# Kernel optimization log

Hardware: AMD Instinct MI355X
Metric: run time of the kernel (lower is better)

The kernel has to match this reference:

```python
import jax, jax.numpy as jnp
import numpy as np

B, TMAX = 16, 30
FEAT = 512   # feat_chans
RNN = 512    # rnn_units == embedding_units (required by the module's wiring)
ATTN = 512   # attention_units
VOCAB = 110  # vocab_size; embedding/output have VOCAB+1 entries
H, W = 8, 64


def setup_inputs() -> dict:
    key = jax.random.key(0)
    ks = jax.random.split(key, 20)
    s = 0.02
    G = 4 * RNN
    return {
        "features": jax.random.normal(ks[0], (B, FEAT, H, W), jnp.float32),
        "encoded": jax.random.normal(ks[1], (B, RNN), jnp.float32),
        # embedding table: (vocab_size + 1, embedding_units)
        "embed_w": jax.random.normal(ks[2], (VOCAB + 1, RNN), jnp.float32) * s,
        # decoder LSTMCell(embedding_units, rnn_units)
        "dec_Wih": jax.random.normal(ks[3], (G, RNN), jnp.float32) * s,
        "dec_Whh": jax.random.normal(ks[4], (G, RNN), jnp.float32) * s,
        "dec_bih": jnp.zeros((G,), jnp.float32),
        "dec_bhh": jnp.zeros((G,), jnp.float32),
        # attention LSTMCell(feat_chans, rnn_units)
        "att_Wih": jax.random.normal(ks[5], (G, FEAT), jnp.float32) * s,
        "att_Whh": jax.random.normal(ks[6], (G, RNN), jnp.float32) * s,
        "att_bih": jnp.zeros((G,), jnp.float32),
        "att_bhh": jnp.zeros((G,), jnp.float32),
        # feat_conv: Conv2d(feat_chans, attention_units, 3, padding='same')
        "feat_conv_w": jax.random.normal(ks[7], (ATTN, FEAT, 3, 3), jnp.float32) * s,
        "feat_conv_b": jnp.zeros((ATTN,), jnp.float32),
        # state_conv: Conv2d(rnn_units, attention_units, 1, bias=False) -> plain matmul on [B,RNN]
        "state_conv_w": jax.random.normal(ks[8], (ATTN, RNN), jnp.float32) * s,
        # attention_projector: Conv2d(attention_units, 1, 1, bias=False)
        "attn_proj_w": jax.random.normal(ks[9], (ATTN,), jnp.float32) * s,
        # output_dense: Linear(rnn_units, vocab_size + 1)
        "out_w": jax.random.normal(ks[10], (VOCAB + 1, RNN), jnp.float32) * s,
        "out_b": jnp.zeros((VOCAB + 1,), jnp.float32),
        "gt": jax.random.randint(ks[11], (B, TMAX), 0, VOCAB + 1),
    }


def _lstm_cell(x, h, c, Wih, Whh, bih, bhh):
    # PyTorch LSTMCell gate order: i, f, g, o
    gates = x @ Wih.T + bih + h @ Whh.T + bhh
    i, f, g, o = jnp.split(gates, 4, axis=-1)
    c_new = jax.nn.sigmoid(f) * c + jax.nn.sigmoid(i) * jnp.tanh(g)
    h_new = jax.nn.sigmoid(o) * jnp.tanh(c_new)
    return h_new, c_new


def reference(features, encoded, embed_w, dec_Wih, dec_Whh, dec_bih, dec_bhh,
              att_Wih, att_Whh, att_bih, att_bhh,
              feat_conv_w, feat_conv_b, state_conv_w, attn_proj_w,
              out_w, out_b, gt):
    b = features.shape[0]
    hdim = features.shape[2] * features.shape[3]
    zeros = jnp.zeros((b, dec_Whh.shape[1]), features.dtype)
    # decoder LSTM: zero initial state on both calls (second call also omits state)
    h0, c0 = _lstm_cell(encoded, zeros, zeros, dec_Wih, dec_Whh, dec_bih, dec_bhh)
    # (the second decoder lstm call produces hidden_state/cell_state which are
    #  never used downstream, so it does not affect the output)

    # feat_conv is applied to constant features -> hoist out of the time loop
    feat_proj = jax.lax.conv_general_dilated(
        features, feat_conv_w, (1, 1), 'SAME',
        dimension_numbers=('NCHW', 'OIHW', 'NCHW')) + feat_conv_b[None, :, None, None]

    emb = embed_w[gt]  # [B, T, E] teacher-forcing embeddings

    def step(_, emb_t):
        h1, c1 = _lstm_cell(emb_t, h0, c0, att_Wih, att_Whh, att_bih, att_bhh)
        h2, _ = _lstm_cell(h0, h1, c1, att_Wih, att_Whh, att_bih, att_bhh)
        state_proj = h2 @ state_conv_w.T  # [B, ATTN] (1x1 conv on 1x1 map)
        a = jnp.tanh(feat_proj + state_proj[:, :, None, None])  # [B, ATTN, H, W]
        scores = jnp.einsum('bahw,a->bhw', a, attn_proj_w)  # 1x1 conv to 1 chan
        attn = jax.nn.softmax(scores.reshape(b, hdim), axis=-1)
        attn = attn.reshape(scores.shape)
        glimpse = jnp.einsum('bchw,bhw->bc', features, attn)  # [B, FEAT]
        logits = glimpse @ out_w.T + out_b  # dropout with p=0 is identity
        return None, logits

    _, outs = jax.lax.scan(step, None, jnp.swapaxes(emb, 0, 1))  # [T, B, V+1]
    return jnp.swapaxes(outs, 0, 1)  # [B, T, V+1]
```

## Files before the change

kernel.cpp:

```cpp
#include <hip/hip_runtime.h>
#include <hip/hip_bf16.h>
#include <stdint.h>

#define BB 16
#define TMAX 30
#define FEAT 512
#define RNN 512
#define ATTN 512
#define VOCABP1 111
#define HWD 512
#define PH 10
#define PW 66
#define PROWS 660
#define G4 2048
#define NHC 16
#define LSTR 40

typedef unsigned short u16;
typedef __attribute__((ext_vector_type(8))) unsigned short us8v;
typedef __attribute__((ext_vector_type(8))) short short8;
typedef __attribute__((ext_vector_type(4))) float f32x4;

__device__ __forceinline__ float b2f(u16 b){
  unsigned int u = ((unsigned int)b) << 16;
  return __builtin_bit_cast(float, u);
}
__device__ __forceinline__ u16 f2b(float x){
  unsigned int u = __builtin_bit_cast(unsigned int, x);
  unsigned int r = u + 0x7FFFu + ((u >> 16) & 1u);
  return (u16)(r >> 16);
}
__device__ __forceinline__ float fsig(float x){ return __fdividef(1.0f, 1.0f + __expf(-x)); }
__device__ __forceinline__ float ftanhf(float x){ return 1.0f - __fdividef(2.0f, __expf(2.0f*x) + 1.0f); }

__global__ __launch_bounds__(256) void k_prep(const float* __restrict__ feats, const float* __restrict__ fconv_w,
                                              const float* __restrict__ att_Wih, const float* __restrict__ att_Whh,
                                              const float* __restrict__ scw, const float* __restrict__ embw,
                                              u16* __restrict__ featsP, u16* __restrict__ wB,
                                              u16* __restrict__ wAih, u16* __restrict__ wAhh,
                                              u16* __restrict__ wScw, u16* __restrict__ wEmb){
  __shared__ float tile[64*65];
  int blk = blockIdx.x, tid = threadIdx.x;
  if (blk < 1024){
    int hwb = blk & 7, cb = (blk >> 3) & 7, b = blk >> 6;
    int c0 = cb*64, hw0 = hwb*64;
    int tx = tid & 63, ty = tid >> 6;
#pragma unroll
    for (int r = 0; r < 16; ++r){
      int cl = ty*16 + r;
      tile[cl*65 + tx] = feats[((size_t)(b*FEAT + c0 + cl))*HWD + hw0 + tx];
    }
    __syncthreads();
#pragma unroll
    for (int r = 0; r < 16; ++r){
      int hwl = ty*16 + r;
      int hw = hw0 + hwl;
      int rowP = hw + 2*(hw >> 6) + 67;
      featsP[((size_t)b*PROWS + rowP)*FEAT + c0 + tx] = f2b(tile[tx*65 + hwl]);
    }
  } else if (blk < 2048){
    int idx = (blk - 1024)*256 + tid;
#pragma unroll
    for (int j = 0; j < 9; ++j){
      int e = j*262144 + idx;
      int c = e & 511, n = (e >> 9) & 511, k9 = e >> 18;
      wB[e] = f2b(fconv_w[((size_t)(n*512 + c))*9 + k9]);
    }
  } else if (blk < 2560){
    const int T2 = 1048576 + 1048576 + 262144 + VOCABP1*512;
    int gtid = (blk - 2048)*256 + tid;
    for (int e = gtid; e < T2; e += 131072){
      if (e < 1048576)            wAih[e]           = f2b(att_Wih[e]);
      else if (e < 2097152)       wAhh[e - 1048576] = f2b(att_Whh[e - 1048576]);
      else if (e < 2359296)       wScw[e - 2097152] = f2b(scw[e - 2097152]);
      else                        wEmb[e - 2359296] = f2b(embw[e - 2359296]);
    }
  } else {
    int blkl = blk - 2560;
    for (int r = blkl; r < 148*BB; r += 128){
      int b = r / 148, j = r % 148;
      int rowP;
      if (j < 66) rowP = j;
      else if (j < 132) rowP = 594 + (j - 66);
      else if (j < 140) rowP = (j - 132 + 1)*66;
      else rowP = (j - 140 + 1)*66 + 65;
      ((unsigned int*)&featsP[((size_t)b*PROWS + rowP)*FEAT])[tid] = 0u;
    }
  }
}

__global__ __launch_bounds__(256) void k_conv(const u16* __restrict__ featsP, const u16* __restrict__ wB,
                                              const float* __restrict__ bias, float* __restrict__ fpe){
  __shared__ __align__(16) u16 As[128*LSTR];
  __shared__ __align__(16) u16 Bs[64*LSTR];
  int m0 = blockIdx.x * 128, n0 = blockIdx.y * 64;
  int tid = threadIdx.x, lane = tid & 63, wave = tid >> 6;
  int wm = wave >> 1, wn = wave & 1;

  int kk = (lane & 3) * 8;
  int rA0 = 32*wave + (lane >> 2);
  int rA1 = rA0 + 16;
  int mA0 = m0 + rA0, mA1 = m0 + rA1;
  long baseA0 = ((long)((mA0 >> 9)*PH + ((mA0 >> 6) & 7) + 1)*PW + (mA0 & 63) + 1)*FEAT + kk;
  long baseA1 = ((long)((mA1 >> 9)*PH + ((mA1 >> 6) & 7) + 1)*PW + (mA1 & 63) + 1)*FEAT + kk;
  int nloc = 16*wave + (lane >> 2);
  long baseB = (long)(n0 + nloc)*512 + kk;

  f32x4 acc[4][2];
#pragma unroll
  for (int i=0;i<4;++i)
#pragma unroll
    for (int j=0;j<2;++j) acc[i][j] = (f32x4){0.f,0.f,0.f,0.f};

  int arow = wm*64 + (lane & 15);
  int akc  = (lane >> 4) * 8;
  int brow = wn*32 + (lane & 15);

  us8v a0c, a1c, bc;
  {
    long dA = (long)(-1*PW - 1)*FEAT;
    a0c = *(const us8v*)(featsP + baseA0 + dA);
    a1c = *(const us8v*)(featsP + baseA1 + dA);
    bc  = *(const us8v*)(wB + baseB);
  }

  for (int ks = 0; ks < 144; ++ks){
    __syncthreads();
    *(us8v*)&As[rA0*LSTR + kk] = a0c;
    *(us8v*)&As[rA1*LSTR + kk] = a1c;
    *(us8v*)&Bs[nloc*LSTR + kk] = bc;
    __syncthreads();
    if (ks < 143){
      int kn = ks + 1;
      int o = kn >> 4;
      int c0 = (kn & 15) << 5;
      int dy = o/3 - 1, dx = o - (o/3)*3 - 1;
      long dA = (long)(dy*PW + dx)*FEAT + c0;
      long dB = (long)o*(512*512) + c0;
      a0c = *(const us8v*)(featsP + baseA0 + dA);
      a1c = *(const us8v*)(featsP + baseA1 + dA);
      bc  = *(const us8v*)(wB + baseB + dB);
    }
    short8 a[4], bfr[2];
#pragma unroll
    for (int mt=0; mt<4; ++mt) a[mt] = *(const short8*)&As[(arow + mt*16)*LSTR + akc];
#pragma unroll
    for (int nt=0; nt<2; ++nt) bfr[nt] = *(const short8*)&Bs[(brow + nt*16)*LSTR + akc];
#pragma unroll
    for (int mt=0; mt<4; ++mt)
#pragma unroll
      for (int nt=0; nt<2; ++nt)
        acc[mt][nt] = __builtin_amdgcn_mfma_f32_16x16x32_bf16(a[mt], bfr[nt], acc[mt][nt], 0, 0, 0);
  }
  int col = lane & 15;
  int rbase = (lane >> 4) * 4;
#pragma unroll
  for (int mt=0; mt<4; ++mt){
#pragma unroll
    for (int nt=0; nt<2; ++nt){
      int gn = n0 + wn*32 + nt*16 + col;
      float bv = bias[gn];
#pragma unroll
      for (int r=0; r<4; ++r){
        int gm = m0 + wm*64 + mt*16 + rbase + r;
        fpe[(size_t)gm*ATTN + gn] = __expf(2.0f*(acc[mt][nt][r] + bv));
      }
    }
  }
}

template<int MODE, bool EXPOUT>
__global__ __launch_bounds__(256) void k_gemm_mfma(const u16* __restrict__ A, const u16* __restrict__ X,
                                                   const int* __restrict__ gt, float* __restrict__ G, int M){
  __shared__ __align__(16) u16 As[128*LSTR];
  __shared__ __align__(16) u16 Bs[64*LSTR];
  int m0 = blockIdx.x * 128, n0 = blockIdx.y * 64;
  int tid = threadIdx.x, lane = tid & 63, wave = tid >> 6;
  int wm = wave >> 1, wn = wave & 1;

  int kk = (lane & 3) * 8;
  int rA0 = 32*wave + (lane >> 2);
  int rA1 = rA0 + 16;
  const u16* aptr0 = A + (size_t)(m0 + rA0)*512 + kk;
  const u16* aptr1 = A + (size_t)(m0 + rA1)*512 + kk;
  int nloc = 16*wave + (lane >> 2);
  int btc = n0 + nloc; if (btc > 479) btc = 479;
  const u16* bptr;
  if (MODE == 0) bptr = X + (size_t)gt[btc]*512 + kk;
  else           bptr = X + (size_t)btc*512 + kk;

  f32x4 acc[4][2];
#pragma unroll
  for (int i=0;i<4;++i)
#pragma unroll
    for (int j=0;j<2;++j) acc[i][j] = (f32x4){0.f,0.f,0.f,0.f};

  int arow = wm*64 + (lane & 15);
  int akc  = (lane >> 4) * 8;
  int brow = wn*32 + (lane & 15);

  us8v a0c = *(const us8v*)aptr0;
  us8v a1c = *(const us8v*)aptr1;
  us8v bc  = *(const us8v*)bptr;

  for (int ks = 0; ks < 16; ++ks){
    __syncthreads();
    *(us8v*)&As[rA0*LSTR + kk] = a0c;
    *(us8v*)&As[rA1*LSTR + kk] = a1c;
    *(us8v*)&Bs[nloc*LSTR + kk] = bc;
    __syncthreads();
    if (ks < 15){
      int off = (ks + 1)*32;
      a0c = *(const us8v*)(aptr0 + off);
      a1c = *(const us8v*)(aptr1 + off);
      bc  = *(const us8v*)(bptr + off);
    }
    short8 a[4], bfr[2];
#pragma unroll
    for (int mt=0; mt<4; ++mt) a[mt] = *(const short8*)&As[(arow + mt*16)*LSTR + akc];
#pragma unroll
    for (int nt=0; nt<2; ++nt) bfr[nt] = *(const short8*)&Bs[(brow + nt*16)*LSTR + akc];
#pragma unroll
    for (int mt=0; mt<4; ++mt)
#pragma unroll
      for (int nt=0; nt<2; ++nt)
        acc[mt][nt] = __builtin_amdgcn_mfma_f32_16x16x32_bf16(a[mt], bfr[nt], acc[mt][nt], 0, 0, 0);
  }
  int col = lane & 15;
  int rbase = (lane >> 4) * 4;
#pragma unroll
  for (int mt=0; mt<4; ++mt){
#pragma unroll
    for (int nt=0; nt<2; ++nt){
      int gbt = n0 + wn*32 + nt*16 + col;
      if (gbt < 480){
#pragma unroll
        for (int r=0; r<4; ++r){
          int gm = m0 + wm*64 + mt*16 + rbase + r;
          float v = acc[mt][nt][r];
          if (EXPOUT) v = __expf(2.0f*v);
          G[(size_t)gbt*M + gm] = v;
        }
      }
    }
  }
}

__global__ __launch_bounds__(256) void k_dec_gemm(const float* __restrict__ encoded, const float* __restrict__ Wih,
                                                  float* __restrict__ Gd){
  __shared__ float encL[512][16];
  int m0 = blockIdx.x * 64;
  int tid = threadIdx.x;
  for (int p = 0; p < 2; ++p){
    int k = p*256 + tid;
    for (int n = 0; n < 16; ++n) encL[k][n] = encoded[n*512 + k];
  }
  __syncthreads();
  int m_l = tid & 63, ng = tid >> 6;
  float acc[4] = {0.f,0.f,0.f,0.f};
  const float* wrow = Wih + (size_t)(m0 + m_l)*512;
  for (int k = 0; k < 512; k += 4){
    float4 w4 = *(const float4*)&wrow[k];
#pragma unroll
    for (int i=0;i<4;++i){
      int n = ng*4 + i;
      acc[i] += w4.x*encL[k][n] + w4.y*encL[k+1][n] + w4.z*encL[k+2][n] + w4.w*encL[k+3][n];
    }
  }
#pragma unroll
  for (int i=0;i<4;++i) Gd[(size_t)(ng*4+i)*G4 + m0 + m_l] = acc[i];
}

__global__ __launch_bounds__(256) void k_pre_gemm(const float* __restrict__ Gd,
                                                  const float* __restrict__ dbih, const float* __restrict__ dbhh,
                                                  const float* __restrict__ Wih, const float* __restrict__ Whh,
                                                  const float* __restrict__ bih, const float* __restrict__ bhh,
                                                  float* __restrict__ g1h, float* __restrict__ g2x){
  __shared__ float hL[512][16];
  int m0 = blockIdx.x * 64;
  int tid = threadIdx.x;
  for (int i = tid; i < 8192; i += 256){
    int k = i >> 4, n = i & 15;
    float gi = Gd[(size_t)n*G4 + k]        + dbih[k]      + dbhh[k];
    float gg = Gd[(size_t)n*G4 + k + 1024] + dbih[k+1024] + dbhh[k+1024];
    float go = Gd[(size_t)n*G4 + k + 1536] + dbih[k+1536] + dbhh[k+1536];
    float cv = fsig(gi)*ftanhf(gg);
    hL[k][n] = fsig(go)*ftanhf(cv);
  }
  __syncthreads();
  int m_l = tid & 63, ng = tid >> 6;
  int m = m0 + m_l;
  float a1[4] = {0.f,0.f,0.f,0.f}, a2[4] = {0.f,0.f,0.f,0.f};
  const float* w1 = Whh + (size_t)m*512;
  const float* w2 = Wih + (size_t)m*512;
  for (int k = 0; k < 512; k += 4){
    float4 v1 = *(const float4*)&w1[k];
    float4 v2 = *(const float4*)&w2[k];
#pragma unroll
    for (int i=0;i<4;++i){
      int n = ng*4 + i;
      float x0 = hL[k][n], x1 = hL[k+1][n], x2 = hL[k+2][n], x3 = hL[k+3][n];
      a1[i] += v1.x*x0 + v1.y*x1 + v1.z*x2 + v1.w*x3;
      a2[i] += v2.x*x0 + v2.y*x1 + v2.z*x2 + v2.w*x3;
    }
  }
  float bb = bih[m] + bhh[m];
#pragma unroll
  for (int i=0;i<4;++i){
    g1h[(size_t)(ng*4+i)*G4 + m] = a1[i] + bb;
    g2x[(size_t)(ng*4+i)*G4 + m] = a2[i] + bb;
  }
}

__global__ __launch_bounds__(512) void k_lstm1(const float* __restrict__ G1, const float* __restrict__ g1h,
                                               const float* __restrict__ Gd,
                                               const float* __restrict__ dbih, const float* __restrict__ dbhh,
                                               u16* __restrict__ h1b, float* __restrict__ c1){
  int bt = blockIdx.x, b = bt / TMAX, u = threadIdx.x;
  float dgi = Gd[(size_t)b*G4 + u]        + dbih[u]      + dbhh[u];
  float dgg = Gd[(size_t)b*G4 + u + 1024] + dbih[u+1024] + dbhh[u+1024];
  float c0v = fsig(dgi)*ftanhf(dgg);
  float gi_ = G1[(size_t)bt*G4 + u]        + g1h[(size_t)b*G4 + u];
  float gf  = G1[(size_t)bt*G4 + u + 512]  + g1h[(size_t)b*G4 + u + 512];
  float gg  = G1[(size_t)bt*G4 + u + 1024] + g1h[(size_t)b*G4 + u + 1024];
  float go  = G1[(size_t)bt*G4 + u + 1536] + g1h[(size_t)b*G4 + u + 1536];
  float cv = fsig(gf)*c0v + fsig(gi_)*ftanhf(gg);
  float hv = fsig(go)*ftanhf(cv);
  h1b[(size_t)bt*RNN + u] = f2b(hv); c1[(size_t)bt*RNN + u] = cv;
}
__global__ __launch_bounds__(512) void k_lstm2(const float* __restrict__ G2, const float* __restrict__ g2x,
                                               const float* __restrict__ c1, u16* __restrict__ h2b){
  int bt = blockIdx.x, b = bt / TMAX, u = threadIdx.x;
  float gi_ = G2[(size_t)bt*G4 + u]        + g2x[(size_t)b*G4 + u];
  float gf  = G2[(size_t)bt*G4 + u + 512]  + g2x[(size_t)b*G4 + u + 512];
  float gg  = G2[(size_t)bt*G4 + u + 1024] + g2x[(size_t)b*G4 + u + 1024];
  float go  = G2[(size_t)bt*G4 + u + 1536] + g2x[(size_t)b*G4 + u + 1536];
  float cv = fsig(gf)*c1[(size_t)bt*RNN+u] + fsig(gi_)*ftanhf(gg);
  float hv = fsig(go)*ftanhf(cv);
  h2b[(size_t)bt*RNN + u] = f2b(hv);
}

__global__ __launch_bounds__(512) void k_sc(const float* __restrict__ fpe, const float* __restrict__ spe,
                                            const float* __restrict__ apw, float* __restrict__ sc){
  __shared__ float spL[8][516];
  __shared__ float w2L[512];
  int b = blockIdx.x, hw0 = blockIdx.y * 32, t0 = blockIdx.z * 8;
  int tid = threadIdx.x, lane = tid & 63, wave = tid >> 6;
  for (int i = tid; i < 8*512; i += 512){
    int t = i >> 9, a = i & 511;
    int tg = t0 + t;
    spL[t][a] = (tg < TMAX) ? spe[((size_t)(b*TMAX + tg))*ATTN + a] : 0.f;
  }
  w2L[tid] = -2.0f * apw[tid];
  __syncthreads();
#pragma unroll
  for (int r = 0; r < 4; ++r){
    int row = hw0 + wave*4 + r;
    const float* frow = fpe + ((size_t)b*HWD + row)*ATTN;
    float acc[8];
#pragma unroll
    for (int t=0;t<8;++t) acc[t] = 0.f;
#pragma unroll
    for (int a0 = 0; a0 < 8; ++a0){
      int a = a0*64 + lane;
      float ef = frow[a];
      float w2 = w2L[a];
#pragma unroll
      for (int t=0;t<8;++t){
        float d = __builtin_fmaf(ef, spL[t][a], 1.0f);
        acc[t] = __builtin_fmaf(w2, __builtin_amdgcn_rcpf(d), acc[t]);
      }
    }
#pragma unroll
    for (int t=0;t<8;++t){
      float s = acc[t];
#pragma unroll
      for (int off = 32; off; off >>= 1) s += __shfl_xor(s, off);
      if (lane == 0 && (t0 + t) < TMAX) sc[((size_t)(b*TMAX + t0 + t))*HWD + row] = s;
    }
  }
}

__global__ __launch_bounds__(256) void k_smax(const float* __restrict__ sc, float* __restrict__ attn){
  __shared__ float red[256];
  int bt = blockIdx.x, tid = threadIdx.x;
  float v0 = sc[(size_t)bt*HWD + tid], v1 = sc[(size_t)bt*HWD + tid + 256];
  red[tid] = fmaxf(v0, v1); __syncthreads();
  for (int sd=128; sd; sd>>=1){ if (tid < sd) red[tid] = fmaxf(red[tid], red[tid+sd]); __syncthreads(); }
  float mx = red[0]; __syncthreads();
  float e0 = __expf(v0-mx), e1 = __expf(v1-mx);
  red[tid] = e0+e1; __syncthreads();
  for (int sd=128; sd; sd>>=1){ if (tid < sd) red[tid] += red[tid+sd]; __syncthreads(); }
  float inv = __fdividef(1.0f, red[0]);
  attn[(size_t)bt*HWD + tid]     = e0*inv;
  attn[(size_t)bt*HWD + tid+256] = e1*inv;
}

__global__ __launch_bounds__(512) void k_glimpse(const float* __restrict__ attn, const u16* __restrict__ featsP,
                                                 float* __restrict__ gpart){
  __shared__ float atL[TMAX][32];
  int b = blockIdx.x, hc = blockIdx.y;
  int hw0 = hc*32;
  int tid = threadIdx.x;
  for (int i = tid; i < TMAX*32; i += 512){
    int t = i >> 5, hw = i & 31;
    atL[t][hw] = attn[((size_t)(b*TMAX + t))*HWD + hw0 + hw];
  }
  __syncthreads();
  float acc[TMAX];
#pragma unroll
  for (int t=0;t<TMAX;++t) acc[t] = 0.f;
  const u16* fb = featsP + (size_t)b*PROWS*FEAT;
  for (int hw = 0; hw < 32; ++hw){
    int hwg = hw0 + hw;
    int rowP = hwg + 2*(hwg >> 6) + 67;
    float f = b2f(fb[(size_t)rowP*FEAT + tid]);
#pragma unroll
    for (int t=0;t<TMAX;++t) acc[t] = __builtin_fmaf(f, atL[t][hw], acc[t]);
  }
#pragma unroll
  for (int t = 0; t < TMAX; ++t)
    gpart[(((size_t)hc*BB + b)*TMAX + t)*FEAT + tid] = acc[t];
}

__global__ __launch_bounds__(512) void k_logits(const float* __restrict__ gpart,
                                                const float* __restrict__ outw, const float* __restrict__ outb,
                                                float* __restrict__ out){
  __shared__ float gl[512];
  __shared__ float part[4][128];
  int bt = blockIdx.x, b = bt / TMAX, t = bt % TMAX;
  int tid = threadIdx.x;
  float g = 0.f;
#pragma unroll
  for (int p = 0; p < NHC; ++p)
    g += gpart[(((size_t)p*BB + b)*TMAX + t)*FEAT + tid];
  gl[tid] = g;
  __syncthreads();
  int vg = tid >> 7, v = tid & 127;
  int vv = v < VOCABP1 ? v : VOCABP1-1;
  const float* wr = outw + (size_t)vv*512 + vg*128;
  float s = 0.f;
  for (int k = 0; k < 128; k += 4){
    float4 w4 = *(const float4*)&wr[k];
    s += w4.x*gl[vg*128+k] + w4.y*gl[vg*128+k+1] + w4.z*gl[vg*128+k+2] + w4.w*gl[vg*128+k+3];
  }
  part[vg][v] = s;
  __syncthreads();
  if (tid < VOCABP1)
    out[(size_t)bt*VOCABP1 + tid] = part[0][tid] + part[1][tid] + part[2][tid] + part[3][tid] + outb[tid];
}

extern "C" void kernel_launch(void* const* d_in, const int* in_sizes, int n_in,
                              void* d_out, int out_size, void* d_ws, size_t ws_size,
                              hipStream_t stream){
  (void)in_sizes; (void)n_in; (void)out_size; (void)ws_size;
  const float* features = (const float*)d_in[0];
  const float* encoded  = (const float*)d_in[1];
  const float* embed_w  = (const float*)d_in[2];
  const float* dec_Wih  = (const float*)d_in[3];
  const float* dec_bih  = (const float*)d_in[5];
  const float* dec_bhh  = (const float*)d_in[6];
  const float* att_Wih  = (const float*)d_in[7];
  const float* att_Whh  = (const float*)d_in[8];
  const float* att_bih  = (const float*)d_in[9];
  const float* att_bhh  = (const float*)d_in[10];
  const float* fconv_w  = (const float*)d_in[11];
  const float* fconv_b  = (const float*)d_in[12];
  const float* scw      = (const float*)d_in[13];
  const float* apw      = (const float*)d_in[14];
  const float* outw     = (const float*)d_in[15];
  const float* outb     = (const float*)d_in[16];
  const int* gt         = (const int*)d_in[17];

  char* ws = (char*)d_ws;
  u16*  featsP = (u16*)(ws + 0);
  u16*  wB     = (u16*)(ws + 10813440);
  float* fpe   = (float*)(ws + 15532032);
  u16*  wAih   = (u16*)(ws + 32309248);
  u16*  wAhh   = (u16*)(ws + 34406400);
  u16*  wScw   = (u16*)(ws + 36503552);
  u16*  wEmb   = (u16*)(ws + 37027840);
  float* Gd    = (float*)(ws + 37141504);
  float* g1h   = (float*)(ws + 37272576);
  float* g2x   = (float*)(ws + 37403648);
  float* G1    = (float*)(ws + 37534720);
  u16*  h1b    = (u16*)(ws + 41466880);
  float* c1    = (float*)(ws + 41958400);
  u16*  h2b    = (u16*)(ws + 42941440);
  float* spe   = (float*)(ws + 43432960);
  float* sc    = (float*)(ws + 44416000);
  float* attn  = (float*)(ws + 45399040);
  float* gpart = fpe;

  k_prep<<<dim3(2688), 256, 0, stream>>>(features, fconv_w, att_Wih, att_Whh, scw, embed_w,
                                         featsP, wB, wAih, wAhh, wScw, wEmb);
  k_conv<<<dim3(64,8), 256, 0, stream>>>(featsP, wB, fconv_b, fpe);

  k_dec_gemm<<<dim3(32), 256, 0, stream>>>(encoded, dec_Wih, Gd);
  k_pre_gemm<<<dim3(32), 256, 0, stream>>>(Gd, dec_bih, dec_bhh, att_Wih, att_Whh, att_bih, att_bhh, g1h, g2x);

  k_gemm_mfma<0,false><<<dim3(16,8), 256, 0, stream>>>(wAih, wEmb, gt, G1, G4);
  k_lstm1<<<dim3(480), 512, 0, stream>>>(G1, g1h, Gd, dec_bih, dec_bhh, h1b, c1);
  k_gemm_mfma<1,false><<<dim3(16,8), 256, 0, stream>>>(wAhh, h1b, nullptr, G1, G4);
  k_lstm2<<<dim3(480), 512, 0, stream>>>(G1, g2x, c1, h2b);
  k_gemm_mfma<1,true><<<dim3(4,8), 256, 0, stream>>>(wScw, h2b, nullptr, spe, ATTN);

  k_sc<<<dim3(16,16,4), 512, 0, stream>>>(fpe, spe, apw, sc);
  k_smax<<<dim3(480), 256, 0, stream>>>(sc, attn);
  k_glimpse<<<dim3(16,NHC), 512, 0, stream>>>(attn, featsP, gpart);
  k_logits<<<dim3(480), 512, 0, stream>>>(gpart, outw, outb, (float*)d_out);
}
```

Before: 365.5 us.

## Fuse LSTM gates into GEMM epilogues and merge tail kernels

Attention-LSTM weights are repacked into gate-interleaved, K-concatenated [Wih|Whh] matrices so each LSTM cell becomes one GEMM whose epilogue applies the gate nonlinearities directly. This removes the G1 gate buffers and the separate lstm kernels. The decoder initial-state GEMM moves into the prep kernel, and the conv runs in the same launch as the first LSTM GEMM so the two overlap. Softmax, glimpse and logits are fused into one per-(b,t) kernel, which recomputes the glimpse over all 512 positions per block instead of reusing features across timesteps. LDS stride padding (40 to 32) is dropped, which may add bank conflicts.

```diff
diff --git a/kernel.cpp b/kernel.cpp
--- a/kernel.cpp
+++ b/kernel.cpp
@@ -12,9 +12,6 @@
 #define PH 10
 #define PW 66
 #define PROWS 660
-#define G4 2048
-#define NHC 16
-#define LSTR 40
 
 typedef unsigned short u16;
 typedef __attribute__((ext_vector_type(8))) unsigned short us8v;
@@ -33,22 +30,27 @@
 __device__ __forceinline__ float fsig(float x){ return __fdividef(1.0f, 1.0f + __expf(-x)); }
 __device__ __forceinline__ float ftanhf(float x){ return 1.0f - __fdividef(2.0f, __expf(2.0f*x) + 1.0f); }
 
-__global__ __launch_bounds__(256) void k_prep(const float* __restrict__ feats, const float* __restrict__ fconv_w,
-                                              const float* __restrict__ att_Wih, const float* __restrict__ att_Whh,
-                                              const float* __restrict__ scw, const float* __restrict__ embw,
-                                              u16* __restrict__ featsP, u16* __restrict__ wB,
-                                              u16* __restrict__ wAih, u16* __restrict__ wAhh,
-                                              u16* __restrict__ wScw, u16* __restrict__ wEmb){
+__global__ __launch_bounds__(256) void k_prep(
+    const float* __restrict__ feats, const float* __restrict__ fconv_w,
+    const float* __restrict__ att_Wih, const float* __restrict__ att_Whh,
+    const float* __restrict__ scw, const float* __restrict__ embw,
+    const float* __restrict__ att_bih, const float* __restrict__ att_bhh,
+    const float* __restrict__ encoded, const float* __restrict__ dec_Wih,
+    const float* __restrict__ dec_bih, const float* __restrict__ dec_bhh,
+    u16* __restrict__ featsP, u16* __restrict__ wB,
+    u16* __restrict__ wA1, u16* __restrict__ wA2,
+    u16* __restrict__ wScw, u16* __restrict__ wEmb, float* __restrict__ bsumI,
+    u16* __restrict__ h0b, float* __restrict__ c0){
   __shared__ float tile[64*65];
   int blk = blockIdx.x, tid = threadIdx.x;
   if (blk < 1024){
     int hwb = blk & 7, cb = (blk >> 3) & 7, b = blk >> 6;
-    int c0 = cb*64, hw0 = hwb*64;
+    int c0_ = cb*64, hw0 = hwb*64;
     int tx = tid & 63, ty = tid >> 6;
 #pragma unroll
     for (int r = 0; r < 16; ++r){
       int cl = ty*16 + r;
-      tile[cl*65 + tx] = feats[((size_t)(b*FEAT + c0 + cl))*HWD + hw0 + tx];
+      tile[cl*65 + tx] = feats[((size_t)(b*FEAT + c0_ + cl))*HWD + hw0 + tx];
     }
     __syncthreads();
 #pragma unroll
@@ -56,7 +58,7 @@
       int hwl = ty*16 + r;
       int hw = hw0 + hwl;
       int rowP = hw + 2*(hw >> 6) + 67;
-      featsP[((size_t)b*PROWS + rowP)*FEAT + c0 + tx] = f2b(tile[tx*65 + hwl]);
+      featsP[((size_t)b*PROWS + rowP)*FEAT + c0_ + tx] = f2b(tile[tx*65 + hwl]);
     }
   } else if (blk < 2048){
     int idx = (blk - 1024)*256 + tid;
@@ -67,15 +69,26 @@
       wB[e] = f2b(fconv_w[((size_t)(n*512 + c))*9 + k9]);
     }
   } else if (blk < 2560){
-    const int T2 = 1048576 + 1048576 + 262144 + VOCABP1*512;
     int gtid = (blk - 2048)*256 + tid;
-    for (int e = gtid; e < T2; e += 131072){
-      if (e < 1048576)            wAih[e]           = f2b(att_Wih[e]);
-      else if (e < 2097152)       wAhh[e - 1048576] = f2b(att_Whh[e - 1048576]);
-      else if (e < 2359296)       wScw[e - 2097152] = f2b(scw[e - 2097152]);
-      else                        wEmb[e - 2359296] = f2b(embw[e - 2359296]);
-    }
-  } else {
+    for (int e = gtid; e < 2097152; e += 131072){
+      int mp = e >> 10, k = e & 1023;
+      int u = mp >> 2, g = mp & 3;
+      int row = u + 512*g;
+      if (k < 512){
+        wA1[e] = f2b(att_Wih[(size_t)row*512 + k]);
+        wA2[e] = f2b(att_Whh[(size_t)row*512 + k]);
+      } else {
+        wA1[e] = f2b(att_Whh[(size_t)row*512 + k - 512]);
+        wA2[e] = f2b(att_Wih[(size_t)row*512 + k - 512]);
+      }
+    }
+    for (int e = gtid; e < 262144; e += 131072) wScw[e] = f2b(scw[e]);
+    if (gtid < VOCABP1*512) wEmb[gtid] = f2b(embw[gtid]);
+    if (gtid < 2048){
+      int u = gtid >> 2, g = gtid & 3, row = u + 512*g;
+      bsumI[gtid] = att_bih[row] + att_bhh[row];
+    }
+  } else if (blk < 2688){
     int blkl = blk - 2560;
     for (int r = blkl; r < 148*BB; r += 128){
       int b = r / 148, j = r % 148;
@@ -86,66 +99,221 @@
       else rowP = (j - 140 + 1)*66 + 65;
       ((unsigned int*)&featsP[((size_t)b*PROWS + rowP)*FEAT])[tid] = 0u;
     }
-  }
-}
-
-__global__ __launch_bounds__(256) void k_conv(const u16* __restrict__ featsP, const u16* __restrict__ wB,
-                                              const float* __restrict__ bias, float* __restrict__ fpe){
-  __shared__ __align__(16) u16 As[128*LSTR];
-  __shared__ __align__(16) u16 Bs[64*LSTR];
-  int m0 = blockIdx.x * 128, n0 = blockIdx.y * 64;
+  } else {
+    int b = blk - 2688;
+    for (int i = tid; i < 512; i += 256) tile[i] = encoded[b*512 + i];
+    __syncthreads();
+#pragma unroll
+    for (int p = 0; p < 2; ++p){
+      int u = p*256 + tid;
+      float ai = 0.f, ag = 0.f, ao = 0.f;
+      const float* wi = dec_Wih + (size_t)u*512;
+      const float* wg = dec_Wih + (size_t)(u + 1024)*512;
+      const float* wo = dec_Wih + (size_t)(u + 1536)*512;
+      for (int k = 0; k < 512; k += 4){
+        float x0 = tile[k], x1 = tile[k+1], x2 = tile[k+2], x3 = tile[k+3];
+        float4 a4 = *(const float4*)&wi[k]; ai += a4.x*x0 + a4.y*x1 + a4.z*x2 + a4.w*x3;
+        float4 b4 = *(const float4*)&wg[k]; ag += b4.x*x0 + b4.y*x1 + b4.z*x2 + b4.w*x3;
+        float4 c4 = *(const float4*)&wo[k]; ao += c4.x*x0 + c4.y*x1 + c4.z*x2 + c4.w*x3;
+      }
+      float gi = ai + dec_bih[u]      + dec_bhh[u];
+      float gg = ag + dec_bih[u+1024] + dec_bhh[u+1024];
+      float go = ao + dec_bih[u+1536] + dec_bhh[u+1536];
+      float cv = fsig(gi)*ftanhf(gg);
+      float hv = fsig(go)*ftanhf(cv);
+      c0[b*512 + u] = cv;
+      h0b[b*512 + u] = f2b(hv);
+    }
+  }
+}
+
+__global__ __launch_bounds__(256) void k_conv_gemm1(
+    const u16* __restrict__ featsP, const u16* __restrict__ wB,
+    const float* __restrict__ bias, float* __restrict__ fpe,
+    const u16* __restrict__ wA1, const u16* __restrict__ wEmb,
+    const u16* __restrict__ h0b, const int* __restrict__ gt,
+    const float* __restrict__ bsumI, const float* __restrict__ c0,
+    u16* __restrict__ h1b, float* __restrict__ c1){
+  __shared__ __align__(16) u16 As[128*32];
+  __shared__ __align__(16) u16 Bs[64*32];
+  int blk = blockIdx.x;
   int tid = threadIdx.x, lane = tid & 63, wave = tid >> 6;
   int wm = wave >> 1, wn = wave & 1;
-
-  int kk = (lane & 3) * 8;
+  int kk = (lane & 3)*8;
   int rA0 = 32*wave + (lane >> 2);
   int rA1 = rA0 + 16;
-  int mA0 = m0 + rA0, mA1 = m0 + rA1;
-  long baseA0 = ((long)((mA0 >> 9)*PH + ((mA0 >> 6) & 7) + 1)*PW + (mA0 & 63) + 1)*FEAT + kk;
-  long baseA1 = ((long)((mA1 >> 9)*PH + ((mA1 >> 6) & 7) + 1)*PW + (mA1 & 63) + 1)*FEAT + kk;
   int nloc = 16*wave + (lane >> 2);
-  long baseB = (long)(n0 + nloc)*512 + kk;
-
+  int arow = wm*64 + (lane & 15);
+  int akc  = (lane >> 4)*8;
+  int brow = wn*32 + (lane & 15);
   f32x4 acc[4][2];
 #pragma unroll
   for (int i=0;i<4;++i)
 #pragma unroll
     for (int j=0;j<2;++j) acc[i][j] = (f32x4){0.f,0.f,0.f,0.f};
-
-  int arow = wm*64 + (lane & 15);
-  int akc  = (lane >> 4) * 8;
-  int brow = wn*32 + (lane & 15);
-
-  us8v a0c, a1c, bc;
-  {
-    long dA = (long)(-1*PW - 1)*FEAT;
-    a0c = *(const us8v*)(featsP + baseA0 + dA);
-    a1c = *(const us8v*)(featsP + baseA1 + dA);
-    bc  = *(const us8v*)(wB + baseB);
-  }
-
-  for (int ks = 0; ks < 144; ++ks){
-    __syncthreads();
-    *(us8v*)&As[rA0*LSTR + kk] = a0c;
-    *(us8v*)&As[rA1*LSTR + kk] = a1c;
-    *(us8v*)&Bs[nloc*LSTR + kk] = bc;
-    __syncthreads();
-    if (ks < 143){
-      int kn = ks + 1;
-      int o = kn >> 4;
-      int c0 = (kn & 15) << 5;
-      int dy = o/3 - 1, dx = o - (o/3)*3 - 1;
-      long dA = (long)(dy*PW + dx)*FEAT + c0;
-      long dB = (long)o*(512*512) + c0;
+  int col = lane & 15;
+  int rbase = (lane >> 4)*4;
+
+  if (blk < 512){
+    int m0 = (blk & 63)*128, n0 = (blk >> 6)*64;
+    int mA0 = m0 + rA0, mA1 = m0 + rA1;
+    long baseA0 = ((long)((mA0 >> 9)*PH + ((mA0 >> 6) & 7) + 1)*PW + (mA0 & 63) + 1)*FEAT + kk;
+    long baseA1 = ((long)((mA1 >> 9)*PH + ((mA1 >> 6) & 7) + 1)*PW + (mA1 & 63) + 1)*FEAT + kk;
+    long baseB = (long)(n0 + nloc)*512 + kk;
+    us8v a0c, a1c, bc;
+    {
+      long dA = (long)(-1*PW - 1)*FEAT;
       a0c = *(const us8v*)(featsP + baseA0 + dA);
       a1c = *(const us8v*)(featsP + baseA1 + dA);
-      bc  = *(const us8v*)(wB + baseB + dB);
+      bc  = *(const us8v*)(wB + baseB);
+    }
+    for (int ks = 0; ks < 144; ++ks){
+      __syncthreads();
+      *(us8v*)&As[rA0*32 + kk] = a0c;
+      *(us8v*)&As[rA1*32 + kk] = a1c;
+      *(us8v*)&Bs[nloc*32 + kk] = bc;
+      __syncthreads();
+      if (ks < 143){
+        int kn = ks + 1;
+        int o = kn >> 4;
+        int c0_ = (kn & 15) << 5;
+        int dy = o/3 - 1, dx = o - (o/3)*3 - 1;
+        long dA = (long)(dy*PW + dx)*FEAT + c0_;
+        long dB = (long)o*(512*512) + c0_;
+        a0c = *(const us8v*)(featsP + baseA0 + dA);
+        a1c = *(const us8v*)(featsP + baseA1 + dA);
+        bc  = *(const us8v*)(wB + baseB + dB);
+      }
+      short8 a[4], bfr[2];
+#pragma unroll
+      for (int mt=0; mt<4; ++mt) a[mt] = *(const short8*)&As[(arow + mt*16)*32 + akc];
+#pragma unroll
+      for (int nt=0; nt<2; ++nt) bfr[nt] = *(const short8*)&Bs[(brow + nt*16)*32 + akc];
+#pragma unroll
+      for (int mt=0; mt<4; ++mt)
+#pragma unroll
+        for (int nt=0; nt<2; ++nt)
+          acc[mt][nt] = __builtin_amdgcn_mfma_f32_16x16x32_bf16(a[mt], bfr[nt], acc[mt][nt], 0, 0, 0);
+    }
+#pragma unroll
+    for (int mt=0; mt<4; ++mt){
+#pragma unroll
+      for (int nt=0; nt<2; ++nt){
+        int gn = n0 + wn*32 + nt*16 + col;
+        float bv = bias[gn];
+#pragma unroll
+        for (int r=0; r<4; ++r){
+          int gm = m0 + wm*64 + mt*16 + rbase + r;
+          fpe[(size_t)gm*ATTN + gn] = __expf(2.0f*(acc[mt][nt][r] + bv));
+        }
+      }
+    }
+  } else {
+    int b2 = blk - 512;
+    int m0 = (b2 & 15)*128, n0 = (b2 >> 4)*64;
+    const u16* aptr0 = wA1 + (size_t)(m0 + rA0)*1024 + kk;
+    const u16* aptr1 = wA1 + (size_t)(m0 + rA1)*1024 + kk;
+    int btc = n0 + nloc; if (btc > 479) btc = 479;
+    const u16* bp1 = wEmb + (size_t)gt[btc]*512 + kk;
+    const u16* bp2 = h0b + (size_t)(btc/TMAX)*512 + kk;
+    us8v a0c = *(const us8v*)aptr0;
+    us8v a1c = *(const us8v*)aptr1;
+    us8v bc  = *(const us8v*)bp1;
+    for (int ks = 0; ks < 32; ++ks){
+      __syncthreads();
+      *(us8v*)&As[rA0*32 + kk] = a0c;
+      *(us8v*)&As[rA1*32 + kk] = a1c;
+      *(us8v*)&Bs[nloc*32 + kk] = bc;
+      __syncthreads();
+      if (ks < 31){
+        int kn = ks + 1;
+        int off = kn*32;
+        a0c = *(const us8v*)(aptr0 + off);
+        a1c = *(const us8v*)(aptr1 + off);
+        bc  = (kn < 16) ? *(const us8v*)(bp1 + off) : *(const us8v*)(bp2 + off - 512);
+      }
+      short8 a[4], bfr[2];
+#pragma unroll
+      for (int mt=0; mt<4; ++mt) a[mt] = *(const short8*)&As[(arow + mt*16)*32 + akc];
+#pragma unroll
+      for (int nt=0; nt<2; ++nt) bfr[nt] = *(const short8*)&Bs[(brow + nt*16)*32 + akc];
+#pragma unroll
+      for (int mt=0; mt<4; ++mt)
+#pragma unroll
+        for (int nt=0; nt<2; ++nt)
+          acc[mt][nt] = __builtin_amdgcn_mfma_f32_16x16x32_bf16(a[mt], bfr[nt], acc[mt][nt], 0, 0, 0);
+    }
+#pragma unroll
+    for (int mt=0; mt<4; ++mt){
+#pragma unroll
+      for (int nt=0; nt<2; ++nt){
+        int gbt = n0 + wn*32 + nt*16 + col;
+        if (gbt < 480){
+          int gm0 = m0 + wm*64 + mt*16 + rbase;
+          int u = gm0 >> 2;
+          float4 bs = *(const float4*)&bsumI[gm0];
+          float vi = acc[mt][nt][0] + bs.x;
+          float vf = acc[mt][nt][1] + bs.y;
+          float vg = acc[mt][nt][2] + bs.z;
+          float vo = acc[mt][nt][3] + bs.w;
+          float cp = c0[(gbt/TMAX)*512 + u];
+          float cv = fsig(vf)*cp + fsig(vi)*ftanhf(vg);
+          float hv = fsig(vo)*ftanhf(cv);
+          h1b[(size_t)gbt*512 + u] = f2b(hv);
+          c1[(size_t)gbt*512 + u] = cv;
+        }
+      }
+    }
+  }
+}
+
+__global__ __launch_bounds__(256) void k_gemm_lstm2(
+    const u16* __restrict__ wA2, const u16* __restrict__ h1bsrc, const u16* __restrict__ h0b,
+    const float* __restrict__ bsumI, const float* __restrict__ c1, u16* __restrict__ h2b){
+  __shared__ __align__(16) u16 As[128*32];
+  __shared__ __align__(16) u16 Bs[64*32];
+  int m0 = blockIdx.x*128, n0 = blockIdx.y*64;
+  int tid = threadIdx.x, lane = tid & 63, wave = tid >> 6;
+  int wm = wave >> 1, wn = wave & 1;
+  int kk = (lane & 3)*8;
+  int rA0 = 32*wave + (lane >> 2);
+  int rA1 = rA0 + 16;
+  int nloc = 16*wave + (lane >> 2);
+  const u16* aptr0 = wA2 + (size_t)(m0 + rA0)*1024 + kk;
+  const u16* aptr1 = wA2 + (size_t)(m0 + rA1)*1024 + kk;
+  int btc = n0 + nloc; if (btc > 479) btc = 479;
+  const u16* bp1 = h1bsrc + (size_t)btc*512 + kk;
+  const u16* bp2 = h0b + (size_t)(btc/TMAX)*512 + kk;
+  f32x4 acc[4][2];
+#pragma unroll
+  for (int i=0;i<4;++i)
+#pragma unroll
+    for (int j=0;j<2;++j) acc[i][j] = (f32x4){0.f,0.f,0.f,0.f};
+  int arow = wm*64 + (lane & 15);
+  int akc  = (lane >> 4)*8;
+  int brow = wn*32 + (lane & 15);
+
+  us8v a0c = *(const us8v*)aptr0;
+  us8v a1c = *(const us8v*)aptr1;
+  us8v bc  = *(const us8v*)bp1;
+  for (int ks = 0; ks < 32; ++ks){
+    __syncthreads();
+    *(us8v*)&As[rA0*32 + kk] = a0c;
+    *(us8v*)&As[rA1*32 + kk] = a1c;
+    *(us8v*)&Bs[nloc*32 + kk] = bc;
+    __syncthreads();
+    if (ks < 31){
+      int kn = ks + 1;
+      int off = kn*32;
+      a0c = *(const us8v*)(aptr0 + off);
+      a1c = *(const us8v*)(aptr1 + off);
+      bc  = (kn < 16) ? *(const us8v*)(bp1 + off) : *(const us8v*)(bp2 + off - 512);
     }
     short8 a[4], bfr[2];
 #pragma unroll
-    for (int mt=0; mt<4; ++mt) a[mt] = *(const short8*)&As[(arow + mt*16)*LSTR + akc];
-#pragma unroll
-    for (int nt=0; nt<2; ++nt) bfr[nt] = *(const short8*)&Bs[(brow + nt*16)*LSTR + akc];
+    for (int mt=0; mt<4; ++mt) a[mt] = *(const short8*)&As[(arow + mt*16)*32 + akc];
+#pragma unroll
+    for (int nt=0; nt<2; ++nt) bfr[nt] = *(const short8*)&Bs[(brow + nt*16)*32 + akc];
 #pragma unroll
     for (int mt=0; mt<4; ++mt)
 #pragma unroll
@@ -153,61 +321,61 @@
         acc[mt][nt] = __builtin_amdgcn_mfma_f32_16x16x32_bf16(a[mt], bfr[nt], acc[mt][nt], 0, 0, 0);
   }
   int col = lane & 15;
-  int rbase = (lane >> 4) * 4;
+  int rbase = (lane >> 4)*4;
 #pragma unroll
   for (int mt=0; mt<4; ++mt){
 #pragma unroll
     for (int nt=0; nt<2; ++nt){
-      int gn = n0 + wn*32 + nt*16 + col;
-      float bv = bias[gn];
-#pragma unroll
-      for (int r=0; r<4; ++r){
-        int gm = m0 + wm*64 + mt*16 + rbase + r;
-        fpe[(size_t)gm*ATTN + gn] = __expf(2.0f*(acc[mt][nt][r] + bv));
-      }
-    }
-  }
-}
-
-template<int MODE, bool EXPOUT>
-__global__ __launch_bounds__(256) void k_gemm_mfma(const u16* __restrict__ A, const u16* __restrict__ X,
-                                                   const int* __restrict__ gt, float* __restrict__ G, int M){
-  __shared__ __align__(16) u16 As[128*LSTR];
-  __shared__ __align__(16) u16 Bs[64*LSTR];
-  int m0 = blockIdx.x * 128, n0 = blockIdx.y * 64;
+      int gbt = n0 + wn*32 + nt*16 + col;
+      if (gbt < 480){
+        int gm0 = m0 + wm*64 + mt*16 + rbase;
+        int u = gm0 >> 2;
+        float4 bs = *(const float4*)&bsumI[gm0];
+        float vi = acc[mt][nt][0] + bs.x;
+        float vf = acc[mt][nt][1] + bs.y;
+        float vg = acc[mt][nt][2] + bs.z;
+        float vo = acc[mt][nt][3] + bs.w;
+        float cp = c1[(size_t)gbt*512 + u];
+        float cv = fsig(vf)*cp + fsig(vi)*ftanhf(vg);
+        float hv = fsig(vo)*ftanhf(cv);
+        h2b[(size_t)gbt*512 + u] = f2b(hv);
+      }
+    }
+  }
+}
+
+__global__ __launch_bounds__(256) void k_gemm_spe(const u16* __restrict__ A, const u16* __restrict__ X,
+                                                  float* __restrict__ G){
+  __shared__ __align__(16) u16 As[128*32];
+  __shared__ __align__(16) u16 Bs[64*32];
+  int m0 = blockIdx.x*128, n0 = blockIdx.y*64;
   int tid = threadIdx.x, lane = tid & 63, wave = tid >> 6;
   int wm = wave >> 1, wn = wave & 1;
-
-  int kk = (lane & 3) * 8;
+  int kk = (lane & 3)*8;
   int rA0 = 32*wave + (lane >> 2);
   int rA1 = rA0 + 16;
+  int nloc = 16*wave + (lane >> 2);
   const u16* aptr0 = A + (size_t)(m0 + rA0)*512 + kk;
   const u16* aptr1 = A + (size_t)(m0 + rA1)*512 + kk;
-  int nloc = 16*wave + (lane >> 2);
   int btc = n0 + nloc; if (btc > 479) btc = 479;
-  const u16* bptr;
-  if (MODE == 0) bptr = X + (size_t)gt[btc]*512 + kk;
-  else           bptr = X + (size_t)btc*512 + kk;
-
+  const u16* bptr = X + (size_t)btc*512 + kk;
   f32x4 acc[4][2];
 #pragma unroll
   for (int i=0;i<4;++i)
 #pragma unroll
     for (int j=0;j<2;++j) acc[i][j] = (f32x4){0.f,0.f,0.f,0.f};
-
   int arow = wm*64 + (lane & 15);
-  int akc  = (lane >> 4) * 8;
+  int akc  = (lane >> 4)*8;
   int brow = wn*32 + (lane & 15);
 
   us8v a0c = *(const us8v*)aptr0;
   us8v a1c = *(const us8v*)aptr1;
   us8v bc  = *(const us8v*)bptr;
-
   for (int ks = 0; ks < 16; ++ks){
     __syncthreads();
-    *(us8v*)&As[rA0*LSTR + kk] = a0c;
-    *(us8v*)&As[rA1*LSTR + kk] = a1c;
-    *(us8v*)&Bs[nloc*LSTR + kk] = bc;
+    *(us8v*)&As[rA0*32 + kk] = a0c;
+    *(us8v*)&As[rA1*32 + kk] = a1c;
+    *(us8v*)&Bs[nloc*32 + kk] = bc;
     __syncthreads();
     if (ks < 15){
       int off = (ks + 1)*32;
@@ -217,9 +385,9 @@
     }
     short8 a[4], bfr[2];
 #pragma unroll
-    for (int mt=0; mt<4; ++mt) a[mt] = *(const short8*)&As[(arow + mt*16)*LSTR + akc];
-#pragma unroll
-    for (int nt=0; nt<2; ++nt) bfr[nt] = *(const short8*)&Bs[(brow + nt*16)*LSTR + akc];
+    for (int mt=0; mt<4; ++mt) a[mt] = *(const short8*)&As[(arow + mt*16)*32 + akc];
+#pragma unroll
+    for (int nt=0; nt<2; ++nt) bfr[nt] = *(const short8*)&Bs[(brow + nt*16)*32 + akc];
 #pragma unroll
     for (int mt=0; mt<4; ++mt)
 #pragma unroll
@@ -227,7 +395,7 @@
         acc[mt][nt] = __builtin_amdgcn_mfma_f32_16x16x32_bf16(a[mt], bfr[nt], acc[mt][nt], 0, 0, 0);
   }
   int col = lane & 15;
-  int rbase = (lane >> 4) * 4;
+  int rbase = (lane >> 4)*4;
 #pragma unroll
   for (int mt=0; mt<4; ++mt){
 #pragma unroll
@@ -237,107 +405,11 @@
 #pragma unroll
         for (int r=0; r<4; ++r){
           int gm = m0 + wm*64 + mt*16 + rbase + r;
-          float v = acc[mt][nt][r];
-          if (EXPOUT) v = __expf(2.0f*v);
-          G[(size_t)gbt*M + gm] = v;
+          G[(size_t)gbt*512 + gm] = __expf(2.0f*acc[mt][nt][r]);
         }
       }
     }
   }
-}
-
-__global__ __launch_bounds__(256) void k_dec_gemm(const float* __restrict__ encoded, const float* __restrict__ Wih,
-                                                  float* __restrict__ Gd){
-  __shared__ float encL[512][16];
-  int m0 = blockIdx.x * 64;
-  int tid = threadIdx.x;
-  for (int p = 0; p < 2; ++p){
-    int k = p*256 + tid;
-    for (int n = 0; n < 16; ++n) encL[k][n] = encoded[n*512 + k];
-  }
-  __syncthreads();
-  int m_l = tid & 63, ng = tid >> 6;
-  float acc[4] = {0.f,0.f,0.f,0.f};
-  const float* wrow = Wih + (size_t)(m0 + m_l)*512;
-  for (int k = 0; k < 512; k += 4){
-    float4 w4 = *(const float4*)&wrow[k];
-#pragma unroll
-    for (int i=0;i<4;++i){
-      int n = ng*4 + i;
-      acc[i] += w4.x*encL[k][n] + w4.y*encL[k+1][n] + w4.z*encL[k+2][n] + w4.w*encL[k+3][n];
-    }
-  }
-#pragma unroll
-  for (int i=0;i<4;++i) Gd[(size_t)(ng*4+i)*G4 + m0 + m_l] = acc[i];
-}
-
-__global__ __launch_bounds__(256) void k_pre_gemm(const float* __restrict__ Gd,
-                                                  const float* __restrict__ dbih, const float* __restrict__ dbhh,
-                                                  const float* __restrict__ Wih, const float* __restrict__ Whh,
-                                                  const float* __restrict__ bih, const float* __restrict__ bhh,
-                                                  float* __restrict__ g1h, float* __restrict__ g2x){
-  __shared__ float hL[512][16];
-  int m0 = blockIdx.x * 64;
-  int tid = threadIdx.x;
-  for (int i = tid; i < 8192; i += 256){
-    int k = i >> 4, n = i & 15;
-    float gi = Gd[(size_t)n*G4 + k]        + dbih[k]      + dbhh[k];
-    float gg = Gd[(size_t)n*G4 + k + 1024] + dbih[k+1024] + dbhh[k+1024];
-    float go = Gd[(size_t)n*G4 + k + 1536] + dbih[k+1536] + dbhh[k+1536];
-    float cv = fsig(gi)*ftanhf(gg);
-    hL[k][n] = fsig(go)*ftanhf(cv);
-  }
-  __syncthreads();
-  int m_l = tid & 63, ng = tid >> 6;
-  int m = m0 + m_l;
-  float a1[4] = {0.f,0.f,0.f,0.f}, a2[4] = {0.f,0.f,0.f,0.f};
-  const float* w1 = Whh + (size_t)m*512;
-  const float* w2 = Wih + (size_t)m*512;
-  for (int k = 0; k < 512; k += 4){
-    float4 v1 = *(const float4*)&w1[k];
-    float4 v2 = *(const float4*)&w2[k];
-#pragma unroll
-    for (int i=0;i<4;++i){
-      int n = ng*4 + i;
-      float x0 = hL[k][n], x1 = hL[k+1][n], x2 = hL[k+2][n], x3 = hL[k+3][n];
-      a1[i] += v1.x*x0 + v1.y*x1 + v1.z*x2 + v1.w*x3;
-      a2[i] += v2.x*x0 + v2.y*x1 + v2.z*x2 + v2.w*x3;
-    }
-  }
-  float bb = bih[m] + bhh[m];
-#pragma unroll
-  for (int i=0;i<4;++i){
-    g1h[(size_t)(ng*4+i)*G4 + m] = a1[i] + bb;
-    g2x[(size_t)(ng*4+i)*G4 + m] = a2[i] + bb;
-  }
-}
-
-__global__ __launch_bounds__(512) void k_lstm1(const float* __restrict__ G1, const float* __restrict__ g1h,
-                                               const float* __restrict__ Gd,
-                                               const float* __restrict__ dbih, const float* __restrict__ dbhh,
-                                               u16* __restrict__ h1b, float* __restrict__ c1){
-  int bt = blockIdx.x, b = bt / TMAX, u = threadIdx.x;
-  float dgi = Gd[(size_t)b*G4 + u]        + dbih[u]      + dbhh[u];
-  float dgg = Gd[(size_t)b*G4 + u + 1024] + dbih[u+1024] + dbhh[u+1024];
-  float c0v = fsig(dgi)*ftanhf(dgg);
-  float gi_ = G1[(size_t)bt*G4 + u]        + g1h[(size_t)b*G4 + u];
-  float gf  = G1[(size_t)bt*G4 + u + 512]  + g1h[(size_t)b*G4 + u + 512];
-  float gg  = G1[(size_t)bt*G4 + u + 1024] + g1h[(size_t)b*G4 + u + 1024];
-  float go  = G1[(size_t)bt*G4 + u + 1536] + g1h[(size_t)b*G4 + u + 1536];
-  float cv = fsig(gf)*c0v + fsig(gi_)*ftanhf(gg);
-  float hv = fsig(go)*ftanhf(cv);
-  h1b[(size_t)bt*RNN + u] = f2b(hv); c1[(size_t)bt*RNN + u] = cv;
-}
-__global__ __launch_bounds__(512) void k_lstm2(const float* __restrict__ G2, const float* __restrict__ g2x,
-                                               const float* __restrict__ c1, u16* __restrict__ h2b){
-  int bt = blockIdx.x, b = bt / TMAX, u = threadIdx.x;
-  float gi_ = G2[(size_t)bt*G4 + u]        + g2x[(size_t)b*G4 + u];
-  float gf  = G2[(size_t)bt*G4 + u + 512]  + g2x[(size_t)b*G4 + u + 512];
-  float gg  = G2[(size_t)bt*G4 + u + 1024] + g2x[(size_t)b*G4 + u + 1024];
-  float go  = G2[(size_t)bt*G4 + u + 1536] + g2x[(size_t)b*G4 + u + 1536];
-  float cv = fsig(gf)*c1[(size_t)bt*RNN+u] + fsig(gi_)*ftanhf(gg);
-  float hv = fsig(go)*ftanhf(cv);
-  h2b[(size_t)bt*RNN + u] = f2b(hv);
 }
 
 __global__ __launch_bounds__(512) void k_sc(const float* __restrict__ fpe, const float* __restrict__ spe,
@@ -381,70 +453,53 @@
   }
 }
 
-__global__ __launch_bounds__(256) void k_smax(const float* __restrict__ sc, float* __restrict__ attn){
-  __shared__ float red[256];
-  int bt = blockIdx.x, tid = threadIdx.x;
-  float v0 = sc[(size_t)bt*HWD + tid], v1 = sc[(size_t)bt*HWD + tid + 256];
-  red[tid] = fmaxf(v0, v1); __syncthreads();
-  for (int sd=128; sd; sd>>=1){ if (tid < sd) red[tid] = fmaxf(red[tid], red[tid+sd]); __syncthreads(); }
-  float mx = red[0]; __syncthreads();
-  float e0 = __expf(v0-mx), e1 = __expf(v1-mx);
-  red[tid] = e0+e1; __syncthreads();
-  for (int sd=128; sd; sd>>=1){ if (tid < sd) red[tid] += red[tid+sd]; __syncthreads(); }
-  float inv = __fdividef(1.0f, red[0]);
-  attn[(size_t)bt*HWD + tid]     = e0*inv;
-  attn[(size_t)bt*HWD + tid+256] = e1*inv;
-}
-
-__global__ __launch_bounds__(512) void k_glimpse(const float* __restrict__ attn, const u16* __restrict__ featsP,
-                                                 float* __restrict__ gpart){
-  __shared__ float atL[TMAX][32];
-  int b = blockIdx.x, hc = blockIdx.y;
-  int hw0 = hc*32;
-  int tid = threadIdx.x;
-  for (int i = tid; i < TMAX*32; i += 512){
-    int t = i >> 5, hw = i & 31;
-    atL[t][hw] = attn[((size_t)(b*TMAX + t))*HWD + hw0 + hw];
-  }
-  __syncthreads();
-  float acc[TMAX];
-#pragma unroll
-  for (int t=0;t<TMAX;++t) acc[t] = 0.f;
-  const u16* fb = featsP + (size_t)b*PROWS*FEAT;
-  for (int hw = 0; hw < 32; ++hw){
-    int hwg = hw0 + hw;
-    int rowP = hwg + 2*(hwg >> 6) + 67;
-    float f = b2f(fb[(size_t)rowP*FEAT + tid]);
-#pragma unroll
-    for (int t=0;t<TMAX;++t) acc[t] = __builtin_fmaf(f, atL[t][hw], acc[t]);
-  }
-#pragma unroll
-  for (int t = 0; t < TMAX; ++t)
-    gpart[(((size_t)hc*BB + b)*TMAX + t)*FEAT + tid] = acc[t];
-}
-
-__global__ __launch_bounds__(512) void k_logits(const float* __restrict__ gpart,
-                                                const float* __restrict__ outw, const float* __restrict__ outb,
-                                                float* __restrict__ out){
+__global__ __launch_bounds__(512) void k_tail(const float* __restrict__ sc, const u16* __restrict__ featsP,
+                                              const float* __restrict__ outw, const float* __restrict__ outb,
+                                              float* __restrict__ out){
+  __shared__ float scL[512];
+  __shared__ float red[8];
   __shared__ float gl[512];
   __shared__ float part[4][128];
-  int bt = blockIdx.x, b = bt / TMAX, t = bt % TMAX;
-  int tid = threadIdx.x;
-  float g = 0.f;
-#pragma unroll
-  for (int p = 0; p < NHC; ++p)
-    g += gpart[(((size_t)p*BB + b)*TMAX + t)*FEAT + tid];
-  gl[tid] = g;
-  __syncthreads();
-  int vg = tid >> 7, v = tid & 127;
-  int vv = v < VOCABP1 ? v : VOCABP1-1;
-  const float* wr = outw + (size_t)vv*512 + vg*128;
-  float s = 0.f;
+  int bt = blockIdx.x, b = bt / TMAX;
+  int tid = threadIdx.x, lane = tid & 63, wave = tid >> 6;
+  float v = sc[(size_t)bt*HWD + tid];
+  float m = v;
+#pragma unroll
+  for (int off = 32; off; off >>= 1) m = fmaxf(m, __shfl_xor(m, off));
+  if (lane == 0) red[wave] = m;
+  __syncthreads();
+  float mx = red[0];
+#pragma unroll
+  for (int i = 1; i < 8; ++i) mx = fmaxf(mx, red[i]);
+  float e = __expf(v - mx);
+  float s = e;
+#pragma unroll
+  for (int off = 32; off; off >>= 1) s += __shfl_xor(s, off);
+  __syncthreads();
+  if (lane == 0) red[wave] = s;
+  __syncthreads();
+  float tot = 0.f;
+#pragma unroll
+  for (int i = 0; i < 8; ++i) tot += red[i];
+  scL[tid] = e * __builtin_amdgcn_rcpf(tot);
+  __syncthreads();
+  const u16* fb = featsP + (size_t)b*PROWS*FEAT;
+  float acc = 0.f;
+  for (int hw = 0; hw < HWD; ++hw){
+    int rowP = hw + 2*(hw >> 6) + 67;
+    acc = __builtin_fmaf(b2f(fb[(size_t)rowP*FEAT + tid]), scL[hw], acc);
+  }
+  gl[tid] = acc;
+  __syncthreads();
+  int vg = tid >> 7, vv = tid & 127;
+  int vc = vv < VOCABP1 ? vv : VOCABP1-1;
+  const float* wr = outw + (size_t)vc*512 + vg*128;
+  float so = 0.f;
   for (int k = 0; k < 128; k += 4){
     float4 w4 = *(const float4*)&wr[k];
-    s += w4.x*gl[vg*128+k] + w4.y*gl[vg*128+k+1] + w4.z*gl[vg*128+k+2] + w4.w*gl[vg*128+k+3];
-  }
-  part[vg][v] = s;
+    so += w4.x*gl[vg*128+k] + w4.y*gl[vg*128+k+1] + w4.z*gl[vg*128+k+2] + w4.w*gl[vg*128+k+3];
+  }
+  part[vg][vv] = so;
   __syncthreads();
   if (tid < VOCABP1)
     out[(size_t)bt*VOCABP1 + tid] = part[0][tid] + part[1][tid] + part[2][tid] + part[3][tid] + outb[tid];
@@ -476,37 +531,26 @@
   u16*  featsP = (u16*)(ws + 0);
   u16*  wB     = (u16*)(ws + 10813440);
   float* fpe   = (float*)(ws + 15532032);
-  u16*  wAih   = (u16*)(ws + 32309248);
-  u16*  wAhh   = (u16*)(ws + 34406400);
-  u16*  wScw   = (u16*)(ws + 36503552);
-  u16*  wEmb   = (u16*)(ws + 37027840);
-  float* Gd    = (float*)(ws + 37141504);
-  float* g1h   = (float*)(ws + 37272576);
-  float* g2x   = (float*)(ws + 37403648);
-  float* G1    = (float*)(ws + 37534720);
-  u16*  h1b    = (u16*)(ws + 41466880);
-  float* c1    = (float*)(ws + 41958400);
-  u16*  h2b    = (u16*)(ws + 42941440);
-  float* spe   = (float*)(ws + 43432960);
-  float* sc    = (float*)(ws + 44416000);
-  float* attn  = (float*)(ws + 45399040);
-  float* gpart = fpe;
-
-  k_prep<<<dim3(2688), 256, 0, stream>>>(features, fconv_w, att_Wih, att_Whh, scw, embed_w,
-                                         featsP, wB, wAih, wAhh, wScw, wEmb);
-  k_conv<<<dim3(64,8), 256, 0, stream>>>(featsP, wB, fconv_b, fpe);
-
-  k_dec_gemm<<<dim3(32), 256, 0, stream>>>(encoded, dec_Wih, Gd);
-  k_pre_gemm<<<dim3(32), 256, 0, stream>>>(Gd, dec_bih, dec_bhh, att_Wih, att_Whh, att_bih, att_bhh, g1h, g2x);
-
-  k_gemm_mfma<0,false><<<dim3(16,8), 256, 0, stream>>>(wAih, wEmb, gt, G1, G4);
-  k_lstm1<<<dim3(480), 512, 0, stream>>>(G1, g1h, Gd, dec_bih, dec_bhh, h1b, c1);
-  k_gemm_mfma<1,false><<<dim3(16,8), 256, 0, stream>>>(wAhh, h1b, nullptr, G1, G4);
-  k_lstm2<<<dim3(480), 512, 0, stream>>>(G1, g2x, c1, h2b);
-  k_gemm_mfma<1,true><<<dim3(4,8), 256, 0, stream>>>(wScw, h2b, nullptr, spe, ATTN);
-
+  u16*  wA1    = (u16*)(ws + 32309248);
+  u16*  wA2    = (u16*)(ws + 36503552);
+  u16*  wScw   = (u16*)(ws + 40697856);
+  u16*  wEmb   = (u16*)(ws + 41222144);
+  float* bsumI = (float*)(ws + 41335808);
+  u16*  h0b    = (u16*)(ws + 41344000);
+  float* c0    = (float*)(ws + 41360384);
+  u16*  h1b    = (u16*)(ws + 41393152);
+  float* c1    = (float*)(ws + 41884672);
+  u16*  h2b    = (u16*)(ws + 42867712);
+  float* spe   = (float*)(ws + 43359232);
+  float* sc    = (float*)(ws + 44342272);
+
+  k_prep<<<dim3(2704), 256, 0, stream>>>(features, fconv_w, att_Wih, att_Whh, scw, embed_w,
+                                         att_bih, att_bhh, encoded, dec_Wih, dec_bih, dec_bhh,
+                                         featsP, wB, wA1, wA2, wScw, wEmb, bsumI, h0b, c0);
+  k_conv_gemm1<<<dim3(640), 256, 0, stream>>>(featsP, wB, fconv_b, fpe,
+                                              wA1, wEmb, h0b, gt, bsumI, c0, h1b, c1);
+  k_gemm_lstm2<<<dim3(16,8), 256, 0, stream>>>(wA2, h1b, h0b, bsumI, c1, h2b);
+  k_gemm_spe<<<dim3(4,8), 256, 0, stream>>>(wScw, h2b, spe);
   k_sc<<<dim3(16,16,4), 512, 0, stream>>>(fpe, spe, apw, sc);
-  k_smax<<<dim3(480), 256, 0, stream>>>(sc, attn);
-  k_glimpse<<<dim3(16,NHC), 512, 0, stream>>>(attn, featsP, gpart);
-  k_logits<<<dim3(480), 512, 0, stream>>>(gpart, outw, outb, (float*)d_out);
-}
+  k_tail<<<dim3(480), 512, 0, stream>>>(sc, featsP, outw, outb, (float*)d_out);
+}
```

New measurement: 379.5 us. 1.04x slower.
